# Optimization experiments

Measured on AMD Instinct MI355X. Metric: run time of the kernel, lower is better.

Reference implementation:

```python
import jax, jax.numpy as jnp
import numpy as np

B, S, D, H = 4, 2048, 1024, 16
DK = D // H  # 64


def setup_inputs() -> dict:
    key = jax.random.key(0)
    ks = jax.random.split(key, 7)
    scale = 1.0 / np.sqrt(D)
    q = jax.random.normal(ks[0], (B, S, D), dtype=jnp.float32)
    k = jax.random.normal(ks[1], (B, S, D), dtype=jnp.float32)
    v = jax.random.normal(ks[2], (B, S, D), dtype=jnp.float32)
    # causal mask, broadcastable to [B, H, S, S]
    mask = jnp.tril(jnp.ones((S, S), dtype=jnp.int32))[None, None, :, :]
    Wq = jax.random.normal(ks[3], (D, D), dtype=jnp.float32) * scale
    Wk = jax.random.normal(ks[4], (D, D), dtype=jnp.float32) * scale
    Wv = jax.random.normal(ks[5], (D, D), dtype=jnp.float32) * scale
    Wo = jax.random.normal(ks[6], (D, D), dtype=jnp.float32) * scale
    return {"q": q, "k": k, "v": v, "mask": mask,
            "Wq": Wq, "Wk": Wk, "Wv": Wv, "Wo": Wo}


def reference(q, k, v, mask, Wq, Wk, Wv, Wo):
    # nn.Linear(bias=False): y = x @ W.T
    query = jnp.einsum('bsd,ed->bse', q, Wq).reshape(B, S, H, DK).transpose(0, 2, 1, 3)
    key_ = jnp.einsum('bsd,ed->bse', k, Wk).reshape(B, S, H, DK).transpose(0, 2, 1, 3)
    value = jnp.einsum('bsd,ed->bse', v, Wv).reshape(B, S, H, DK).transpose(0, 2, 1, 3)
    scores = jnp.einsum('bhqd,bhkd->bhqk', query, key_) / jnp.sqrt(jnp.float32(DK))
    scores = jnp.where(mask == 0, -jnp.inf, scores)
    probs = jax.nn.softmax(scores, axis=-1)
    x = jnp.einsum('bhqk,bhkd->bhqd', probs, value)  # [B,H,S,DK]
    x = x.transpose(0, 2, 1, 3).reshape(B, S, D)
    return jnp.einsum('bsd,ed->bse', x, Wo)
```

## Files before the change

kernel.cpp:

```cpp
#include <hip/hip_runtime.h>
#include <hip/hip_bf16.h>

constexpr int Bn = 4, Sn = 2048, Dn = 1024, Hn = 16, DKn = 64;
constexpr int Mrows = Bn * Sn;
constexpr int NQB = Sn / 64;

typedef __attribute__((ext_vector_type(8))) short short8;
typedef __attribute__((ext_vector_type(4))) float f32x4;
typedef __attribute__((ext_vector_type(4))) unsigned int u32x4;

#define DEV __device__ __forceinline__

constexpr float QSCL = 0.18033688f;

DEV unsigned short f2bf(float f) {
    unsigned u = __builtin_bit_cast(unsigned, f);
    u += 0x7FFFu + ((u >> 16) & 1u);
    return (unsigned short)(u >> 16);
}
DEV unsigned pk2(float a, float b) {
    __hip_bfloat162 h = __float22bfloat162_rn(float2{a, b});
    unsigned u;
    __builtin_memcpy(&u, &h, 4);
    return u;
}
DEV float exp2a(float x) {
    float r;
    asm("v_exp_f32 %0, %1" : "=v"(r) : "v"(x));
    return r;
}

__global__ __launch_bounds__(256) void cvt_w(const float* __restrict__ W0,
                                             const float* __restrict__ W1,
                                             const float* __restrict__ W2,
                                             const float* __restrict__ W3,
                                             unsigned short* __restrict__ Out) {
    const float* src = blockIdx.y == 0 ? W0
                     : blockIdx.y == 1 ? W1
                     : blockIdx.y == 2 ? W2 : W3;
    size_t off = ((size_t)blockIdx.x * 256 + threadIdx.x) * 8;
    const float4* s = (const float4*)(src + off);
    float4 a = s[0], b = s[1];
    u32x4 p = {pk2(a.x, a.y), pk2(a.z, a.w), pk2(b.x, b.y), pk2(b.z, b.w)};
    *(u32x4*)(Out + (size_t)blockIdx.y * (Dn * Dn) + off) = p;
}

template <bool ABF16, bool BBF16, bool OUTF32>
DEV void gemm_body(const void* __restrict__ Ap, const void* __restrict__ Bw,
                   void* __restrict__ Out, float oscale) {
    __shared__ alignas(16) unsigned short As[128 * 72];
    __shared__ alignas(16) unsigned short Bs[128 * 72];

    const int tid = threadIdx.x;
    const int bid = (int)(blockIdx.y * gridDim.x + blockIdx.x);
    const int xcd = bid & 7;
    const int jj = bid >> 3;
    const int m0 = (xcd + ((jj & 7) << 3)) * 128;
    const int n0 = (jj >> 3) * 128;
    const int lane = tid & 63;
    const int w = tid >> 6;
    const int wm = (w >> 1) * 32;
    const int wn = (w & 1) * 64;
    const int g = lane >> 4, q15 = lane & 15;

    f32x4 acc[2][4] = {};

    const int srow = tid >> 2, sseg = tid & 3;

    const float* Af = (const float*)Ap;
    const unsigned short* Ab = (const unsigned short*)Ap;
    const float* Bf = (const float*)Bw;
    const unsigned short* Bb = (const unsigned short*)Bw;

    float4 fa[4], fb[4];
    u32x4 ua[2], ub[2];

    auto loadA = [&](int kk) {
        if constexpr (ABF16) {
            const u32x4* s =
                (const u32x4*)(Ab + (size_t)(m0 + srow) * Dn + kk + sseg * 16);
            ua[0] = s[0];
            ua[1] = s[1];
        } else {
            const float4* s =
                (const float4*)(Af + (size_t)(m0 + srow) * Dn + kk + sseg * 16);
            fa[0] = s[0]; fa[1] = s[1]; fa[2] = s[2]; fa[3] = s[3];
        }
    };
    auto loadB = [&](int kk) {
        if constexpr (BBF16) {
            const u32x4* s =
                (const u32x4*)(Bb + (size_t)(n0 + srow) * Dn + kk + sseg * 16);
            ub[0] = s[0];
            ub[1] = s[1];
        } else {
            const float4* s =
                (const float4*)(Bf + (size_t)(n0 + srow) * Dn + kk + sseg * 16);
            fb[0] = s[0]; fb[1] = s[1]; fb[2] = s[2]; fb[3] = s[3];
        }
    };
    auto store = [&]() {
        u32x4* da = (u32x4*)(&As[srow * 72 + sseg * 16]);
        if constexpr (ABF16) {
            da[0] = ua[0];
            da[1] = ua[1];
        } else {
            u32x4 p0 = {pk2(fa[0].x, fa[0].y), pk2(fa[0].z, fa[0].w),
                        pk2(fa[1].x, fa[1].y), pk2(fa[1].z, fa[1].w)};
            u32x4 p1 = {pk2(fa[2].x, fa[2].y), pk2(fa[2].z, fa[2].w),
                        pk2(fa[3].x, fa[3].y), pk2(fa[3].z, fa[3].w)};
            da[0] = p0;
            da[1] = p1;
        }
        u32x4* db = (u32x4*)(&Bs[srow * 72 + sseg * 16]);
        if constexpr (BBF16) {
            db[0] = ub[0];
            db[1] = ub[1];
        } else {
            u32x4 q0 = {pk2(fb[0].x, fb[0].y), pk2(fb[0].z, fb[0].w),
                        pk2(fb[1].x, fb[1].y), pk2(fb[1].z, fb[1].w)};
            u32x4 q1 = {pk2(fb[2].x, fb[2].y), pk2(fb[2].z, fb[2].w),
                        pk2(fb[3].x, fb[3].y), pk2(fb[3].z, fb[3].w)};
            db[0] = q0;
            db[1] = q1;
        }
    };

    loadA(0);
    loadB(0);
    for (int kk = 0; kk < Dn; kk += 64) {
        store();
        __syncthreads();
        if (kk + 64 < Dn) {
            loadA(kk + 64);
            loadB(kk + 64);
        }

#pragma unroll
        for (int ks = 0; ks < 2; ++ks) {
            short8 af[2], bf4[4];
#pragma unroll
            for (int mf = 0; mf < 2; ++mf)
                af[mf] = __builtin_bit_cast(
                    short8, *(const u32x4*)(&As[(wm + mf * 16 + q15) * 72 +
                                                ks * 32 + g * 8]));
#pragma unroll
            for (int nf = 0; nf < 4; ++nf)
                bf4[nf] = __builtin_bit_cast(
                    short8, *(const u32x4*)(&Bs[(wn + nf * 16 + q15) * 72 +
                                                ks * 32 + g * 8]));
#pragma unroll
            for (int mf = 0; mf < 2; ++mf)
#pragma unroll
                for (int nf = 0; nf < 4; ++nf)
                    acc[mf][nf] = __builtin_amdgcn_mfma_f32_16x16x32_bf16(
                        af[mf], bf4[nf], acc[mf][nf], 0, 0, 0);
        }
        __syncthreads();
    }

#pragma unroll
    for (int mf = 0; mf < 2; ++mf)
#pragma unroll
        for (int nf = 0; nf < 4; ++nf)
#pragma unroll
            for (int r = 0; r < 4; ++r) {
                int m = m0 + wm + mf * 16 + 4 * g + r;
                int n = n0 + wn + nf * 16 + q15;
                float val = acc[mf][nf][r] * oscale;
                if (OUTF32) {
                    ((float*)Out)[(size_t)m * Dn + n] = val;
                } else {
                    int b = m >> 11, s = m & (Sn - 1);
                    int h = n >> 6, dk = n & 63;
                    ((unsigned short*)Out)[(((size_t)(b * Hn + h) * Sn + s) << 6) +
                                           dk] = f2bf(val);
                }
            }
}

template <bool ABF16, bool BBF16, bool OUTF32>
__global__ __launch_bounds__(512) void gemm_nt(const void* __restrict__ Ap,
                                               const void* __restrict__ Bw,
                                               void* __restrict__ Out,
                                               float oscale) {
    gemm_body<ABF16, BBF16, OUTF32>(Ap, Bw, Out, oscale);
}

__global__ __launch_bounds__(512) void attn_fwd(
    const unsigned short* __restrict__ Qb, const unsigned short* __restrict__ Kb,
    const unsigned short* __restrict__ Vb, unsigned short* __restrict__ Xb) {
    __shared__ alignas(16) unsigned short Kt[64 * 64];
    __shared__ alignas(16) unsigned short Vt[64 * 64];

    const int tid = threadIdx.x;
    const int pair = blockIdx.x;
    const int bh = blockIdx.y;
    const int b = bh >> 4, h = bh & 15;
    const int lane = tid & 63, w = tid >> 6;
    const int g = lane >> 4, q15 = lane & 15;

    const unsigned short* Qh = Qb + (size_t)bh * Sn * DKn;
    const unsigned short* Kh = Kb + (size_t)bh * Sn * DKn;
    const unsigned short* Vh = Vb + (size_t)bh * Sn * DKn;

    const int st_row = tid >> 3, st_seg = tid & 7;
    const int sv_kv = tid & 63, sv_g = tid >> 6;
    const int sel = sv_kv & 1;
    const int kv_even = sv_kv & ~1;
    const unsigned kvp = (unsigned)(((kv_even & 32) | ((kv_even & 12) << 1) |
                                     ((kv_even & 16) >> 2) | (kv_even & 3)) *
                                    2);

    const short8 ones = {0x3F80, 0x3F80, 0x3F80, 0x3F80,
                         0x3F80, 0x3F80, 0x3F80, 0x3F80};

    u32x4 kr0, vr0;
    auto load_kv = [&](int j) {
        kr0 = *(const u32x4*)(Kh + (size_t)(j * 64 + st_row) * DKn + st_seg * 8);
        vr0 = *(const u32x4*)(Vh + (size_t)(j * 64 + sv_kv) * DKn + sv_g * 8);
    };

    for (int hp = 0; hp < 2; ++hp) {
        const int c = hp == 0 ? (15 - pair) : pair;
        const int jmax = 2 * c + 1;
        const int jdiag = 2 * c + (w >> 2);
        const int qg = c * 128 + w * 16 + q15;

        short8 qf[2];
#pragma unroll
        for (int ks = 0; ks < 2; ++ks)
            qf[ks] = __builtin_bit_cast(
                short8, *(const u32x4*)(Qh + (size_t)qg * DKn + ks * 32 + g * 8));

        f32x4 xacc[4] = {};
        f32x4 xl = {};
        float m_run = -1e30f;

        load_kv(0);
        for (int j = 0; j <= jmax; ++j) {
            {
                unsigned b0 = ((unsigned)(st_row * 128 + st_seg * 16)) ^
                              ((unsigned)(st_row & 7) << 4);
                *(u32x4*)((char*)Kt + b0) = kr0;
            }
            {
                int dk0 = sv_g * 8;
#pragma unroll
                for (int i = 0; i < 4; ++i) {
                    unsigned mine = vr0[i];
                    unsigned theirs = (unsigned)__shfl_xor((int)mine, 1);
                    int dk_abs = dk0 + 2 * i + sel;
                    unsigned out = sel ? ((theirs >> 16) | (mine & 0xffff0000u))
                                       : ((mine & 0xffffu) | (theirs << 16));
                    unsigned byteoff = ((unsigned)(dk_abs * 128) + kvp) ^
                                       ((unsigned)(dk_abs & 7) << 4);
                    *(unsigned*)((char*)Vt + byteoff) = out;
                }
            }
            __syncthreads();

            if (j < jmax) load_kv(j + 1);

            if (j <= jdiag) {
                f32x4 sacc[4] = {};
#pragma unroll
                for (int mf = 0; mf < 4; ++mf) {
                    int row = mf * 16 + q15;
#pragma unroll
                    for (int ks = 0; ks < 2; ++ks) {
                        unsigned byteoff =
                            ((unsigned)(row * 128 + ks * 64 + g * 16)) ^
                            ((unsigned)(row & 7) << 4);
                        short8 kf = __builtin_bit_cast(
                            short8, *(const u32x4*)((char*)Kt + byteoff));
                        sacc[mf] = __builtin_amdgcn_mfma_f32_16x16x32_bf16(
                            kf, qf[ks], sacc[mf], 0, 0, 0);
                    }
                }

                float p[4][4];
                float pmax = -1e30f;
                const bool diag = (j == jdiag);
#pragma unroll
                for (int mf = 0; mf < 4; ++mf)
#pragma unroll
                    for (int r = 0; r < 4; ++r) {
                        float sv = sacc[mf][r];
                        if (diag) {
                            int kvg = j * 64 + mf * 16 + 4 * g + r;
                            if (kvg > qg) sv = -1e30f;
                        }
                        p[mf][r] = sv;
                        pmax = fmaxf(pmax, sv);
                    }
                pmax = fmaxf(pmax, __shfl_xor(pmax, 16));
                pmax = fmaxf(pmax, __shfl_xor(pmax, 32));
                if (__any(pmax > m_run + 8.f)) {
                    float mnew = fmaxf(m_run, pmax);
                    float corr = exp2a(m_run - mnew);
#pragma unroll
                    for (int mf = 0; mf < 4; ++mf)
#pragma unroll
                        for (int r = 0; r < 4; ++r) xacc[mf][r] *= corr;
#pragma unroll
                    for (int r = 0; r < 4; ++r) xl[r] *= corr;
                    m_run = mnew;
                }
#pragma unroll
                for (int mf = 0; mf < 4; ++mf)
#pragma unroll
                    for (int r = 0; r < 4; ++r)
                        p[mf][r] = exp2a(p[mf][r] - m_run);

                unsigned pkk[4][2];
#pragma unroll
                for (int mf = 0; mf < 4; ++mf) {
                    pkk[mf][0] = pk2(p[mf][0], p[mf][1]);
                    pkk[mf][1] = pk2(p[mf][2], p[mf][3]);
                }
#pragma unroll
                for (int ks = 0; ks < 2; ++ks) {
                    u32x4 tmp = {pkk[2 * ks][0], pkk[2 * ks][1],
                                 pkk[2 * ks + 1][0], pkk[2 * ks + 1][1]};
                    short8 pb = __builtin_bit_cast(short8, tmp);
                    xl = __builtin_amdgcn_mfma_f32_16x16x32_bf16(ones, pb, xl,
                                                                 0, 0, 0);
#pragma unroll
                    for (int mf = 0; mf < 4; ++mf) {
                        int row = mf * 16 + q15;
                        unsigned byteoff =
                            ((unsigned)(row * 128 + ks * 64 + g * 16)) ^
                            ((unsigned)(row & 7) << 4);
                        short8 vf = __builtin_bit_cast(
                            short8, *(const u32x4*)((char*)Vt + byteoff));
                        xacc[mf] = __builtin_amdgcn_mfma_f32_16x16x32_bf16(
                            vf, pb, xacc[mf], 0, 0, 0);
                    }
                }
            }
            __syncthreads();
        }

        float inv = 1.0f / xl[0];
        size_t rowbase = (size_t)(b * Sn + c * 128 + w * 16 + q15) * Dn + h * 64;
#pragma unroll
        for (int mf = 0; mf < 4; ++mf) {
            unsigned w0 = pk2(xacc[mf][0] * inv, xacc[mf][1] * inv);
            unsigned w1 = pk2(xacc[mf][2] * inv, xacc[mf][3] * inv);
            uint2 val = {w0, w1};
            *(uint2*)(Xb + rowbase + mf * 16 + 4 * g) = val;
        }
    }
}

extern "C" void kernel_launch(void* const* d_in, const int* in_sizes, int n_in,
                              void* d_out, int out_size, void* d_ws, size_t ws_size,
                              hipStream_t stream) {
    (void)in_sizes; (void)n_in; (void)out_size;
    const float* q = (const float*)d_in[0];
    const float* k = (const float*)d_in[1];
    const float* v = (const float*)d_in[2];
    const float* Wq = (const float*)d_in[4];
    const float* Wk = (const float*)d_in[5];
    const float* Wv = (const float*)d_in[6];
    const float* Wo = (const float*)d_in[7];

    unsigned short* Qb = (unsigned short*)d_ws;
    unsigned short* Kb = Qb + (size_t)Mrows * Dn;
    unsigned short* Vb = Kb + (size_t)Mrows * Dn;
    unsigned short* Xb = Vb + (size_t)Mrows * Dn;
    unsigned short* Wb = Xb + (size_t)Mrows * Dn;

    const size_t needW =
        (size_t)4 * Mrows * Dn * 2 + (size_t)4 * Dn * Dn * 2;
    const bool useWb = ws_size >= needW;

    dim3 blk(256);
    dim3 gblk(512);
    dim3 ggrid(Dn / 128, Mrows / 128);
    dim3 agrid(NQB / 4, Bn * Hn);

    if (useWb) {
        cvt_w<<<dim3(Dn * Dn / (256 * 8), 4), blk, 0, stream>>>(Wq, Wk, Wv, Wo, Wb);
        const unsigned short* Wqb = Wb;
        const unsigned short* Wkb = Wb + (size_t)Dn * Dn;
        const unsigned short* Wvb = Wb + (size_t)2 * Dn * Dn;
        const unsigned short* Wob = Wb + (size_t)3 * Dn * Dn;
        gemm_nt<false, true, false><<<ggrid, gblk, 0, stream>>>(q, Wqb, Qb, QSCL);
        gemm_nt<false, true, false><<<ggrid, gblk, 0, stream>>>(k, Wkb, Kb, 1.0f);
        gemm_nt<false, true, false><<<ggrid, gblk, 0, stream>>>(v, Wvb, Vb, 1.0f);
        attn_fwd<<<agrid, gblk, 0, stream>>>(Qb, Kb, Vb, Xb);
        gemm_nt<true, true, true><<<ggrid, gblk, 0, stream>>>(Xb, Wob, d_out, 1.0f);
    } else {
        gemm_nt<false, false, false><<<ggrid, gblk, 0, stream>>>(q, Wq, Qb, QSCL);
        gemm_nt<false, false, false><<<ggrid, gblk, 0, stream>>>(k, Wk, Kb, 1.0f);
        gemm_nt<false, false, false><<<ggrid, gblk, 0, stream>>>(v, Wv, Vb, 1.0f);
        attn_fwd<<<agrid, gblk, 0, stream>>>(Qb, Kb, Vb, Xb);
        gemm_nt<true, false, true><<<ggrid, gblk, 0, stream>>>(Xb, Wo, d_out, 1.0f);
    }
}
```

Baseline: 193.6 us.

## Double-buffer GEMM LDS tiles with direct global-to-LDS loads and XOR swizzle

The projection GEMM now keeps two LDS buffers per operand and, for bf16 operands, loads tiles straight from global memory into LDS with global_load_lds instead of going through registers. The padded 72-element row stride is replaced by an XOR swizzle on 16-byte segments to avoid bank conflicts, and the trailing barrier per k-step is removed because the next tile goes to the other buffer. The aim is to overlap loads with MFMA work and cut register staging and barriers. It relies on the wait and barrier ordering for the asynchronous LDS writes being correct, which is the main risk.

Result: slower. 205.8 us (+6.3%).

```diff
diff --git a/kernel.cpp b/kernel.cpp
--- a/kernel.cpp
+++ b/kernel.cpp
@@ -12,6 +12,11 @@
 #define DEV __device__ __forceinline__
 
 constexpr float QSCL = 0.18033688f;
+
+#define GLOAD_LDS16(g, l)                                                     \
+    __builtin_amdgcn_global_load_lds(                                         \
+        (const __attribute__((address_space(1))) void*)(g),                   \
+        (__attribute__((address_space(3))) void*)(l), 16, 0, 0)
 
 DEV unsigned short f2bf(float f) {
     unsigned u = __builtin_bit_cast(unsigned, f);
@@ -48,8 +53,8 @@
 template <bool ABF16, bool BBF16, bool OUTF32>
 DEV void gemm_body(const void* __restrict__ Ap, const void* __restrict__ Bw,
                    void* __restrict__ Out, float oscale) {
-    __shared__ alignas(16) unsigned short As[128 * 72];
-    __shared__ alignas(16) unsigned short Bs[128 * 72];
+    __shared__ alignas(16) unsigned short As[2][128 * 64];
+    __shared__ alignas(16) unsigned short Bs[2][128 * 64];
 
     const int tid = threadIdx.x;
     const int bid = (int)(blockIdx.y * gridDim.x + blockIdx.x);
@@ -65,7 +70,8 @@
 
     f32x4 acc[2][4] = {};
 
-    const int srow = tid >> 2, sseg = tid & 3;
+    const int grow = tid >> 3, gseg = tid & 7;
+    const int srow = tid >> 2, sp = (tid & 3) * 2;
 
     const float* Af = (const float*)Ap;
     const unsigned short* Ab = (const unsigned short*)Ap;
@@ -73,82 +79,94 @@
     const unsigned short* Bb = (const unsigned short*)Bw;
 
     float4 fa[4], fb[4];
-    u32x4 ua[2], ub[2];
-
-    auto loadA = [&](int kk) {
+
+    auto issueA = [&](int kk, int p) {
         if constexpr (ABF16) {
-            const u32x4* s =
-                (const u32x4*)(Ab + (size_t)(m0 + srow) * Dn + kk + sseg * 16);
-            ua[0] = s[0];
-            ua[1] = s[1];
+#pragma unroll
+            for (int i = 0; i < 2; ++i) {
+                int row = i * 64 + grow;
+                int ss = gseg ^ (row & 7);
+                GLOAD_LDS16(Ab + (size_t)(m0 + row) * Dn + kk + ss * 8,
+                            (char*)&As[p][0] + i * 8192 + tid * 16);
+            }
         } else {
             const float4* s =
-                (const float4*)(Af + (size_t)(m0 + srow) * Dn + kk + sseg * 16);
+                (const float4*)(Af + (size_t)(m0 + srow) * Dn + kk + sp * 8);
             fa[0] = s[0]; fa[1] = s[1]; fa[2] = s[2]; fa[3] = s[3];
         }
     };
-    auto loadB = [&](int kk) {
+    auto issueB = [&](int kk, int p) {
         if constexpr (BBF16) {
-            const u32x4* s =
-                (const u32x4*)(Bb + (size_t)(n0 + srow) * Dn + kk + sseg * 16);
-            ub[0] = s[0];
-            ub[1] = s[1];
+#pragma unroll
+            for (int i = 0; i < 2; ++i) {
+                int row = i * 64 + grow;
+                int ss = gseg ^ (row & 7);
+                GLOAD_LDS16(Bb + (size_t)(n0 + row) * Dn + kk + ss * 8,
+                            (char*)&Bs[p][0] + i * 8192 + tid * 16);
+            }
         } else {
             const float4* s =
-                (const float4*)(Bf + (size_t)(n0 + srow) * Dn + kk + sseg * 16);
+                (const float4*)(Bf + (size_t)(n0 + srow) * Dn + kk + sp * 8);
             fb[0] = s[0]; fb[1] = s[1]; fb[2] = s[2]; fb[3] = s[3];
         }
     };
-    auto store = [&]() {
-        u32x4* da = (u32x4*)(&As[srow * 72 + sseg * 16]);
-        if constexpr (ABF16) {
-            da[0] = ua[0];
-            da[1] = ua[1];
-        } else {
+    auto storeRegs = [&](int p) {
+        if constexpr (!ABF16) {
             u32x4 p0 = {pk2(fa[0].x, fa[0].y), pk2(fa[0].z, fa[0].w),
                         pk2(fa[1].x, fa[1].y), pk2(fa[1].z, fa[1].w)};
             u32x4 p1 = {pk2(fa[2].x, fa[2].y), pk2(fa[2].z, fa[2].w),
                         pk2(fa[3].x, fa[3].y), pk2(fa[3].z, fa[3].w)};
-            da[0] = p0;
-            da[1] = p1;
-        }
-        u32x4* db = (u32x4*)(&Bs[srow * 72 + sseg * 16]);
-        if constexpr (BBF16) {
-            db[0] = ub[0];
-            db[1] = ub[1];
-        } else {
+            unsigned b0 = ((unsigned)(srow * 128 + sp * 16)) ^
+                          ((unsigned)(srow & 7) << 4);
+            unsigned b1 = ((unsigned)(srow * 128 + sp * 16 + 16)) ^
+                          ((unsigned)(srow & 7) << 4);
+            *(u32x4*)((char*)&As[p][0] + b0) = p0;
+            *(u32x4*)((char*)&As[p][0] + b1) = p1;
+        }
+        if constexpr (!BBF16) {
             u32x4 q0 = {pk2(fb[0].x, fb[0].y), pk2(fb[0].z, fb[0].w),
                         pk2(fb[1].x, fb[1].y), pk2(fb[1].z, fb[1].w)};
             u32x4 q1 = {pk2(fb[2].x, fb[2].y), pk2(fb[2].z, fb[2].w),
                         pk2(fb[3].x, fb[3].y), pk2(fb[3].z, fb[3].w)};
-            db[0] = q0;
-            db[1] = q1;
+            unsigned b0 = ((unsigned)(srow * 128 + sp * 16)) ^
+                          ((unsigned)(srow & 7) << 4);
+            unsigned b1 = ((unsigned)(srow * 128 + sp * 16 + 16)) ^
+                          ((unsigned)(srow & 7) << 4);
+            *(u32x4*)((char*)&Bs[p][0] + b0) = q0;
+            *(u32x4*)((char*)&Bs[p][0] + b1) = q1;
         }
     };
 
-    loadA(0);
-    loadB(0);
-    for (int kk = 0; kk < Dn; kk += 64) {
-        store();
+    issueA(0, 0);
+    issueB(0, 0);
+    for (int kk = 0, jt = 0; kk < Dn; kk += 64, ++jt) {
+        const int p = jt & 1;
+        storeRegs(p);
         __syncthreads();
         if (kk + 64 < Dn) {
-            loadA(kk + 64);
-            loadB(kk + 64);
+            issueA(kk + 64, p ^ 1);
+            issueB(kk + 64, p ^ 1);
         }
 
 #pragma unroll
         for (int ks = 0; ks < 2; ++ks) {
             short8 af[2], bf4[4];
 #pragma unroll
-            for (int mf = 0; mf < 2; ++mf)
+            for (int mf = 0; mf < 2; ++mf) {
+                int row = wm + mf * 16 + q15;
+                unsigned bo = ((unsigned)(row * 128 + ks * 64 + g * 16)) ^
+                              ((unsigned)(row & 7) << 4);
                 af[mf] = __builtin_bit_cast(
-                    short8, *(const u32x4*)(&As[(wm + mf * 16 + q15) * 72 +
-                                                ks * 32 + g * 8]));
-#pragma unroll
-            for (int nf = 0; nf < 4; ++nf)
+                    short8, *(const u32x4*)((char*)&As[p][0] + bo));
+            }
+#pragma unroll
+            for (int nf = 0; nf < 4; ++nf) {
+                int row = wn + nf * 16 + q15;
+                unsigned bo = ((unsigned)(row * 128 + ks * 64 + g * 16)) ^
+                              ((unsigned)(row & 7) << 4);
                 bf4[nf] = __builtin_bit_cast(
-                    short8, *(const u32x4*)(&Bs[(wn + nf * 16 + q15) * 72 +
-                                                ks * 32 + g * 8]));
+                    short8, *(const u32x4*)((char*)&Bs[p][0] + bo));
+            }
 #pragma unroll
             for (int mf = 0; mf < 2; ++mf)
 #pragma unroll
@@ -156,7 +174,6 @@
                     acc[mf][nf] = __builtin_amdgcn_mfma_f32_16x16x32_bf16(
                         af[mf], bf4[nf], acc[mf][nf], 0, 0, 0);
         }
-        __syncthreads();
     }
 
 #pragma unroll
```
